# Performance work log

Hardware: AMD Instinct MI355X
Metric: run time of the kernel (lower is better)

The kernel has to match this reference:

```python
import jax, jax.numpy as jnp
import numpy as np


def setup_inputs() -> dict:
    key = jax.random.key(0)
    ks = jax.random.split(key, 9)
    B, S, D, E, I = 4, 2048, 1024, 8, 2048
    sd = 1.0 / np.sqrt(D)
    si = 1.0 / np.sqrt(I)
    return {
        "hidden_states": jax.random.normal(ks[0], (B, S, D), dtype=jnp.float32),
        "gate_w": jax.random.normal(ks[1], (D, E), dtype=jnp.float32) * sd,
        "expert_gate_w": jax.random.normal(ks[2], (E, D, I), dtype=jnp.float32) * sd,
        "expert_up_w": jax.random.normal(ks[3], (E, D, I), dtype=jnp.float32) * sd,
        "expert_down_w": jax.random.normal(ks[4], (E, I, D), dtype=jnp.float32) * si,
        "shared_gate_proj_w": jax.random.normal(ks[5], (D, I), dtype=jnp.float32) * sd,
        "shared_up_w": jax.random.normal(ks[6], (D, I), dtype=jnp.float32) * sd,
        "shared_down_w": jax.random.normal(ks[7], (I, D), dtype=jnp.float32) * si,
        "shared_expert_gate_w": jax.random.normal(ks[8], (D, 1), dtype=jnp.float32) * sd,
        "top_k": 2,
    }


def reference(hidden_states, gate_w, expert_gate_w, expert_up_w, expert_down_w,
              shared_gate_proj_w, shared_up_w, shared_down_w, shared_expert_gate_w,
              top_k):
    B, S, D = hidden_states.shape
    E = gate_w.shape[1]
    x = hidden_states.reshape(-1, D)            # [T, D]
    T = x.shape[0]

    # Router: softmax in fp32, top-k, dense per-token per-expert combine weights.
    gate_vals = x @ gate_w                      # [T, E]
    probs = jax.nn.softmax(gate_vals.astype(jnp.float32), axis=-1)
    top_w, top_i = jax.lax.top_k(probs, top_k)  # [T, K]
    dense_w = jnp.zeros((T, E), dtype=jnp.float32)
    dense_w = dense_w.at[jnp.arange(T)[:, None], top_i].set(top_w)
    dense_w = dense_w.astype(x.dtype)           # zero for unselected experts

    # All experts as batched SwiGLU GEMMs (tokens with zero weight contribute 0).
    g = jnp.einsum('td,edi->eti', x, expert_gate_w)
    u = jnp.einsum('td,edi->eti', x, expert_up_w)
    y = jnp.einsum('eti,eid->etd', jax.nn.silu(g) * u, expert_down_w)  # [E, T, D]
    moe_out = jnp.einsum('etd,te->td', y, dense_w)                      # [T, D]

    # Shared expert with sigmoid gate.
    shared = (jax.nn.silu(x @ shared_gate_proj_w) * (x @ shared_up_w)) @ shared_down_w
    shared = jax.nn.sigmoid(x @ shared_expert_gate_w) * shared

    final = (moe_out + shared).reshape(B, S, D)
    return final, gate_vals
```

## Files before the change

kernel.cpp:

```cpp
#include <hip/hip_runtime.h>

typedef __bf16 bf16x8 __attribute__((ext_vector_type(8)));
typedef float f32x4 __attribute__((ext_vector_type(4)));
typedef float f4 __attribute__((ext_vector_type(4)));
typedef unsigned short us8 __attribute__((ext_vector_type(8)));

#define T_TOK 8192
#define DDIM 1024
#define NEXP 8
#define IDIM 2048
#define NCH 1024
#define RROWS 17408
#define ROWS_TOT (T_TOK + RROWS)

__device__ __forceinline__ unsigned short f2bf(float f) {
    unsigned u = __float_as_uint(f);
    u += 0x7fffu + ((u >> 16) & 1u);
    return (unsigned short)(u >> 16);
}

__global__ __launch_bounds__(256) void router_kernel(
    const float* __restrict__ x, const float* __restrict__ gate_w,
    const float* __restrict__ sgw, float* __restrict__ gate_out,
    float* __restrict__ wdense, float* __restrict__ sgout)
{
    __shared__ float lgw[DDIM * NEXP];
    __shared__ float lsg[DDIM];
    int tid = threadIdx.x;
    for (int i = tid; i < (DDIM * NEXP) / 4; i += 256)
        ((f4*)lgw)[i] = ((const f4*)gate_w)[i];
    for (int i = tid; i < DDIM / 4; i += 256)
        ((f4*)lsg)[i] = ((const f4*)sgw)[i];
    __syncthreads();

    int wid = tid >> 6, l = tid & 63;
    int t = blockIdx.x * 4 + wid;

    float acc[NEXP];
#pragma unroll
    for (int e = 0; e < NEXP; e++) acc[e] = 0.f;
    float accs = 0.f;
    const float* xr = x + (size_t)t * DDIM;
#pragma unroll
    for (int j = 0; j < 4; j++) {
        int d0 = j * 256 + l * 4;
        f4 xv = *(const f4*)(xr + d0);
#pragma unroll
        for (int c = 0; c < 4; c++) {
            float xd = xv[c];
            int d = d0 + c;
#pragma unroll
            for (int e = 0; e < NEXP; e++) acc[e] += xd * lgw[d * NEXP + e];
            accs += xd * lsg[d];
        }
    }
#pragma unroll
    for (int off = 32; off > 0; off >>= 1) {
#pragma unroll
        for (int e = 0; e < NEXP; e++) acc[e] += __shfl_xor(acc[e], off);
        accs += __shfl_xor(accs, off);
    }
    if (l == 0) {
        float m = acc[0];
        for (int e = 1; e < NEXP; e++) m = fmaxf(m, acc[e]);
        float p[NEXP], s = 0.f;
        for (int e = 0; e < NEXP; e++) { p[e] = __expf(acc[e] - m); s += p[e]; }
        float inv = 1.f / s;
        int i1 = 0; float b1 = p[0];
        for (int e = 1; e < NEXP; e++) if (p[e] > b1) { b1 = p[e]; i1 = e; }
        int i2 = -1; float b2 = -1.f;
        for (int e = 0; e < NEXP; e++) if (e != i1 && p[e] > b2) { b2 = p[e]; i2 = e; }
        for (int e = 0; e < NEXP; e++) {
            gate_out[(size_t)t * NEXP + e] = acc[e];
            float w = (e == i1) ? b1 * inv : (e == i2) ? b2 * inv : 0.f;
            wdense[(size_t)t * NEXP + e] = w;
        }
        sgout[t] = 1.f / (1.f + __expf(-accs));
    }
}

__global__ __launch_bounds__(256) void bucket_kernel(
    const float* __restrict__ wdense, int* __restrict__ list,
    float* __restrict__ wl, int* __restrict__ cnt,
    int* __restrict__ te, int* __restrict__ tp)
{
    int e = blockIdx.x;
    int tid = threadIdx.x, wid = tid >> 6, l = tid & 63;
    __shared__ int wsum[4];
    int base = 0;
    int* le = list + (size_t)e * T_TOK;
    float* we = wl + (size_t)e * T_TOK;
    for (int t0 = 0; t0 < T_TOK; t0 += 256) {
        int tok = t0 + tid;
        float w = wdense[(size_t)tok * NEXP + e];
        bool f = w > 0.f;
        unsigned long long m = __ballot(f);
        int lp = __popcll(m & ((1ull << l) - 1ull));
        if (l == 0) wsum[wid] = __popcll(m);
        __syncthreads();
        int woff = 0;
#pragma unroll
        for (int i = 0; i < 4; i++) if (i < wid) woff += wsum[i];
        int btot = wsum[0] + wsum[1] + wsum[2] + wsum[3];
        if (f) {
            int pos = base + woff + lp;
            le[pos] = tok; we[pos] = w;
            int slot = 0;
            for (int e2 = 0; e2 < e; e2++)
                slot += (wdense[(size_t)tok * NEXP + e2] > 0.f) ? 1 : 0;
            te[tok * 2 + slot] = e;
            tp[tok * 2 + slot] = pos;
        }
        base += btot;
        __syncthreads();
    }
    if (tid == 0) cnt[e] = base;
    int align = (base + 127) & ~127;
    for (int i = base + tid; i < align; i += 256) { le[i] = 0; we[i] = 0.f; }
}

__global__ void scan_kernel(const int* __restrict__ cnt, int* __restrict__ offs)
{
    if (threadIdx.x == 0) {
        int o = 0;
        for (int e = 0; e < NEXP; e++) { offs[e] = o; o += (cnt[e] + 127) & ~127; }
    }
}

__global__ __launch_bounds__(256) void cvt_kernel(
    const float* __restrict__ in, unsigned short* __restrict__ out, int n8)
{
    int i = blockIdx.x * 256 + threadIdx.x;
    if (i >= n8) return;
    const f4* p = (const f4*)in + (size_t)i * 2;
    f4 a = p[0], b = p[1];
    us8 o;
#pragma unroll
    for (int k = 0; k < 4; k++) { o[k] = f2bf(a[k]); o[4 + k] = f2bf(b[k]); }
    *((us8*)out + i) = o;
}

__global__ __launch_bounds__(256) void wcvt_gu_kernel(
    const float* __restrict__ egw, const float* __restrict__ euw,
    const float* __restrict__ sgp, const float* __restrict__ sup,
    unsigned short* __restrict__ pool, int c0)
{
    int j = blockIdx.y;
    int e = j >> 1, s = j & 1;
    const float* src = (e < 8) ? ((s ? euw : egw) + (size_t)e * DDIM * IDIM)
                               : (s ? sup : sgp);
    unsigned short* dst = pool + (size_t)j * NCH * DDIM;
    int tpc = NCH / 64;
    int tci = blockIdx.x % tpc, tri = blockIdx.x / tpc;
    int r0 = tri * 64;
    int cl0 = tci * 64;
    int cg0 = c0 + cl0;

    __shared__ unsigned short lds[64][72];
    int t = threadIdx.x;
    int tr = t >> 4, tcc = (t & 15) * 4;
#pragma unroll
    for (int jj = 0; jj < 4; jj++) {
        int r = tr + jj * 16;
        f4 v = *(const f4*)(src + (size_t)(r0 + r) * IDIM + cg0 + tcc);
#pragma unroll
        for (int k = 0; k < 4; k++) lds[r][tcc + k] = f2bf(v[k]);
    }
    __syncthreads();
    int orow = t >> 2, ss = t & 3;
    us8 v0, v1;
#pragma unroll
    for (int i = 0; i < 8; i++) {
        v0[i] = lds[ss * 16 + i][orow];
        v1[i] = lds[ss * 16 + 8 + i][orow];
    }
    unsigned short* op = dst + (size_t)(cl0 + orow) * DDIM + r0 + ss * 16;
    *(us8*)op = v0; *(us8*)(op + 8) = v1;
}

__global__ __launch_bounds__(256) void wcvt_d_kernel(
    const float* __restrict__ edw, const float* __restrict__ sdw,
    unsigned short* __restrict__ pool)
{
    int j = blockIdx.y;
    const float* src = (j < 8) ? edw + (size_t)j * IDIM * DDIM : sdw;
    unsigned short* dst = pool + (size_t)j * DDIM * IDIM;
    int tpc = DDIM / 64;
    int tci = blockIdx.x % tpc, tri = blockIdx.x / tpc;
    int rg0 = tri * 64;
    int cg0 = tci * 64;

    __shared__ unsigned short lds[64][72];
    int t = threadIdx.x;
    int tr = t >> 4, tcc = (t & 15) * 4;
#pragma unroll
    for (int jj = 0; jj < 4; jj++) {
        int r = tr + jj * 16;
        f4 v = *(const f4*)(src + (size_t)(rg0 + r) * DDIM + cg0 + tcc);
#pragma unroll
        for (int k = 0; k < 4; k++) lds[r][tcc + k] = f2bf(v[k]);
    }
    __syncthreads();
    int orow = t >> 2, ss = t & 3;
    us8 v0, v1;
#pragma unroll
    for (int i = 0; i < 8; i++) {
        v0[i] = lds[ss * 16 + i][orow];
        v1[i] = lds[ss * 16 + 8 + i][orow];
    }
    unsigned short* op = dst + (size_t)(cg0 + orow) * IDIM + rg0 + ss * 16;
    *(us8*)op = v0; *(us8*)(op + 8) = v1;
}

__device__ __forceinline__ void stage_tile(
    const unsigned short* __restrict__ g, int row0, int ldk, int k0,
    unsigned short* lds, int wid, int lane)
{
#pragma unroll
    for (int j = 0; j < 2; j++) {
        int c = wid + j * 4;
        int seg = c * 64 + lane;
        int row = seg >> 2, ks = seg & 3;
        const unsigned short* gp = g + (size_t)(row0 + row) * ldk + k0 + ks * 8;
        __builtin_amdgcn_global_load_lds(
            (const __attribute__((address_space(1))) void*)gp,
            (__attribute__((address_space(3))) void*)(lds + c * 512),
            16, 0, 0);
    }
}

__global__ __launch_bounds__(256, 2) void gemm_gateup(
    const unsigned short* __restrict__ A, const unsigned short* __restrict__ pool,
    unsigned short* __restrict__ H, const int* __restrict__ listb,
    const int* __restrict__ cnt, const int* __restrict__ offs, int c0)
{
    int z = blockIdx.z;
    const unsigned short *Bg, *Bu; const int* lst; int count, rowb;
    if (z == 0) {
        Bg = pool + (size_t)16 * NCH * DDIM; Bu = pool + (size_t)17 * NCH * DDIM;
        lst = nullptr; count = T_TOK; rowb = 0;
    } else {
        int e = z - 1;
        Bg = pool + (size_t)(e * 2) * NCH * DDIM; Bu = pool + (size_t)(e * 2 + 1) * NCH * DDIM;
        lst = listb + (size_t)e * T_TOK; count = cnt[e]; rowb = T_TOK + offs[e];
    }
    int flat = blockIdx.y * 8 + blockIdx.x;
    int nt = flat & 7, mt = flat >> 3;
    int m0 = mt * 128, n0 = nt * 128;
    if (m0 >= count) return;
    const int K = DDIM;

    __shared__ unsigned short As[128 * 32], Bgs[128 * 32], Bus[128 * 32];
    int tid = threadIdx.x, wid = tid >> 6, l = tid & 63;
    int wm = wid >> 1, wn = wid & 1;
    int lr = l & 15, kg = l >> 4;

    int seg0 = wid * 64 + l, seg1 = (wid + 4) * 64 + l;
    int ra0 = seg0 >> 2, ka0 = seg0 & 3;
    int ra1 = seg1 >> 2, ka1 = seg1 & 3;
    int ga0 = lst ? lst[m0 + ra0] : (m0 + ra0);
    int ga1 = lst ? lst[m0 + ra1] : (m0 + ra1);
    const unsigned short* pa0 = A + (size_t)ga0 * K + ka0 * 8;
    const unsigned short* pa1 = A + (size_t)ga1 * K + ka1 * 8;

    f32x4 zero = {0.f, 0.f, 0.f, 0.f};
    f32x4 accg[4][4], accu[4][4];
#pragma unroll
    for (int m = 0; m < 4; m++)
#pragma unroll
        for (int n = 0; n < 4; n++) { accg[m][n] = zero; accu[m][n] = zero; }

    for (int k0 = 0; k0 < K; k0 += 32) {
        __builtin_amdgcn_global_load_lds(
            (const __attribute__((address_space(1))) void*)(pa0 + k0),
            (__attribute__((address_space(3))) void*)(As + wid * 512), 16, 0, 0);
        __builtin_amdgcn_global_load_lds(
            (const __attribute__((address_space(1))) void*)(pa1 + k0),
            (__attribute__((address_space(3))) void*)(As + (wid + 4) * 512), 16, 0, 0);
        stage_tile(Bg, n0, K, k0, Bgs, wid, l);
        stage_tile(Bu, n0, K, k0, Bus, wid, l);
        __syncthreads();
        bf16x8 a[4], bg[4], bu[4];
#pragma unroll
        for (int m = 0; m < 4; m++)
            a[m] = *(const bf16x8*)(As + ((wm * 64 + m * 16 + lr) * 32 + kg * 8));
#pragma unroll
        for (int n = 0; n < 4; n++) {
            bg[n] = *(const bf16x8*)(Bgs + ((wn * 64 + n * 16 + lr) * 32 + kg * 8));
            bu[n] = *(const bf16x8*)(Bus + ((wn * 64 + n * 16 + lr) * 32 + kg * 8));
        }
#pragma unroll
        for (int m = 0; m < 4; m++)
#pragma unroll
            for (int n = 0; n < 4; n++) {
                accg[m][n] = __builtin_amdgcn_mfma_f32_16x16x32_bf16(a[m], bg[n], accg[m][n], 0, 0, 0);
                accu[m][n] = __builtin_amdgcn_mfma_f32_16x16x32_bf16(a[m], bu[n], accu[m][n], 0, 0, 0);
            }
        __syncthreads();
    }

#pragma unroll
    for (int m = 0; m < 4; m++) {
        int row = rowb + m0 + wm * 64 + m * 16 + kg * 4;
#pragma unroll
        for (int n = 0; n < 4; n++) {
            int col = c0 + n0 + wn * 64 + n * 16 + lr;
#pragma unroll
            for (int r = 0; r < 4; r++) {
                float g = accg[m][n][r], u = accu[m][n][r];
                float hv = g * (1.f / (1.f + __expf(-g))) * u;
                H[(size_t)(row + r) * IDIM + col] = f2bf(hv);
            }
        }
    }
}

__global__ __launch_bounds__(256, 2) void gemm_down(
    const unsigned short* __restrict__ H, const unsigned short* __restrict__ pool,
    unsigned short* __restrict__ Y,
    const float* __restrict__ wlb, const float* __restrict__ sgo,
    const int* __restrict__ cnt, const int* __restrict__ offs)
{
    int z = blockIdx.z;
    const unsigned short* B; const float* coef; int count, rowb;
    if (z == 0) {
        B = pool + (size_t)8 * DDIM * IDIM;
        coef = sgo; count = T_TOK; rowb = 0;
    } else {
        int e = z - 1;
        B = pool + (size_t)e * DDIM * IDIM;
        coef = wlb + (size_t)e * T_TOK;
        count = cnt[e]; rowb = T_TOK + offs[e];
    }
    int flat = blockIdx.y * 8 + blockIdx.x;
    int nt = flat & 7, mt = flat >> 3;
    int m0 = mt * 128, n0 = nt * 128;
    if (m0 >= count) return;
    const unsigned short* Arows = H + (size_t)rowb * IDIM;

    __shared__ unsigned short As[128 * 32], Bs[128 * 32];
    int tid = threadIdx.x, wid = tid >> 6, l = tid & 63;
    int wm = wid >> 1, wn = wid & 1;
    int lr = l & 15, kg = l >> 4;

    f32x4 zero = {0.f, 0.f, 0.f, 0.f};
    f32x4 acc[4][4];
#pragma unroll
    for (int m = 0; m < 4; m++)
#pragma unroll
        for (int n = 0; n < 4; n++) acc[m][n] = zero;

    for (int k0 = 0; k0 < IDIM; k0 += 32) {
        stage_tile(Arows, m0, IDIM, k0, As, wid, l);
        stage_tile(B, n0, IDIM, k0, Bs, wid, l);
        __syncthreads();
        bf16x8 a[4], b[4];
#pragma unroll
        for (int m = 0; m < 4; m++)
            a[m] = *(const bf16x8*)(As + ((wm * 64 + m * 16 + lr) * 32 + kg * 8));
#pragma unroll
        for (int n = 0; n < 4; n++)
            b[n] = *(const bf16x8*)(Bs + ((wn * 64 + n * 16 + lr) * 32 + kg * 8));
#pragma unroll
        for (int m = 0; m < 4; m++)
#pragma unroll
            for (int n = 0; n < 4; n++)
                acc[m][n] = __builtin_amdgcn_mfma_f32_16x16x32_bf16(a[m], b[n], acc[m][n], 0, 0, 0);
        __syncthreads();
    }

#pragma unroll
    for (int m = 0; m < 4; m++) {
        int rloc = m0 + wm * 64 + m * 16 + kg * 4;
        float cf[4];
#pragma unroll
        for (int r = 0; r < 4; r++) cf[r] = coef[rloc + r];
#pragma unroll
        for (int n = 0; n < 4; n++) {
            int col = n0 + wn * 64 + n * 16 + lr;
#pragma unroll
            for (int r = 0; r < 4; r++)
                Y[(size_t)(rowb + rloc + r) * DDIM + col] = f2bf(cf[r] * acc[m][n][r]);
        }
    }
}

__global__ __launch_bounds__(256) void combine_kernel(
    const unsigned short* __restrict__ Y, const int* __restrict__ te,
    const int* __restrict__ tp, const int* __restrict__ offs,
    float* __restrict__ out)
{
    int t = blockIdx.x * 2 + (threadIdx.x >> 7);
    int c = (threadIdx.x & 127) * 8;
    int e0 = te[2 * t], e1 = te[2 * t + 1];
    size_t r0 = (size_t)T_TOK + offs[e0] + tp[2 * t];
    size_t r1 = (size_t)T_TOK + offs[e1] + tp[2 * t + 1];

    us8 vs = *(const us8*)(Y + (size_t)t * DDIM + c);
    us8 v0 = *(const us8*)(Y + r0 * DDIM + c);
    us8 v1 = *(const us8*)(Y + r1 * DDIM + c);
    f4 o0, o1;
#pragma unroll
    for (int k = 0; k < 4; k++) {
        o0[k] = __uint_as_float((unsigned)vs[k] << 16)
              + __uint_as_float((unsigned)v0[k] << 16)
              + __uint_as_float((unsigned)v1[k] << 16);
        o1[k] = __uint_as_float((unsigned)vs[4 + k] << 16)
              + __uint_as_float((unsigned)v0[4 + k] << 16)
              + __uint_as_float((unsigned)v1[4 + k] << 16);
    }
    float* op = out + (size_t)t * DDIM + c;
    *(f4*)op = o0;
    *(f4*)(op + 4) = o1;
}

extern "C" void kernel_launch(void* const* d_in, const int* in_sizes, int n_in,
                              void* d_out, int out_size, void* d_ws, size_t ws_size,
                              hipStream_t stream)
{
    const float* x   = (const float*)d_in[0];
    const float* gw  = (const float*)d_in[1];
    const float* egw = (const float*)d_in[2];
    const float* euw = (const float*)d_in[3];
    const float* edw = (const float*)d_in[4];
    const float* sgp = (const float*)d_in[5];
    const float* sup = (const float*)d_in[6];
    const float* sdw = (const float*)d_in[7];
    const float* seg = (const float*)d_in[8];

    float* out0 = (float*)d_out;
    float* gate_out = out0 + (size_t)T_TOK * DDIM;

    char* ws = (char*)d_ws;
    auto take = [&](size_t bytes) { char* p = ws; ws += (bytes + 255) & ~(size_t)255; return p; };
    unsigned short* xb   = (unsigned short*)take((size_t)T_TOK * DDIM * 2);
    float* wdense = (float*)take((size_t)T_TOK * NEXP * 4);
    float* sgo    = (float*)take((size_t)T_TOK * 4);
    int*   list   = (int*)take((size_t)NEXP * T_TOK * 4);
    float* wl     = (float*)take((size_t)NEXP * T_TOK * 4);
    int*   cnt    = (int*)take(256);
    int*   offs   = (int*)take(256);
    int*   te     = (int*)take((size_t)T_TOK * 2 * 4);
    int*   tp     = (int*)take((size_t)T_TOK * 2 * 4);
    unsigned short* pool = (unsigned short*)take((size_t)18 * NCH * DDIM * 2);
    unsigned short* H    = (unsigned short*)take((size_t)ROWS_TOT * IDIM * 2);
    unsigned short* Y    = (unsigned short*)take((size_t)ROWS_TOT * DDIM * 2);

    router_kernel<<<T_TOK / 4, 256, 0, stream>>>(x, gw, seg, gate_out, wdense, sgo);
    bucket_kernel<<<NEXP, 256, 0, stream>>>(wdense, list, wl, cnt, te, tp);
    scan_kernel<<<1, 64, 0, stream>>>(cnt, offs);
    cvt_kernel<<<(T_TOK * DDIM / 8) / 256, 256, 0, stream>>>(x, xb, T_TOK * DDIM / 8);

    for (int c = 0; c < 2; c++) {
        int c0 = c * NCH;
        wcvt_gu_kernel<<<dim3((NCH / 64) * 16, 18), 256, 0, stream>>>(
            egw, euw, sgp, sup, pool, c0);
        gemm_gateup<<<dim3(8, 64, 9), 256, 0, stream>>>(
            xb, pool, H, list, cnt, offs, c0);
    }

    wcvt_d_kernel<<<dim3((IDIM / 64) * 16, 9), 256, 0, stream>>>(edw, sdw, pool);
    gemm_down<<<dim3(8, 64, 9), 256, 0, stream>>>(H, pool, Y, wl, sgo, cnt, offs);

    combine_kernel<<<T_TOK / 2, 256, 0, stream>>>(Y, te, tp, offs, out0);
}
```

Baseline: 590.8 us.

## Fuse x bf16 conversion into router, drop scan kernel, unchunk gate/up weights

Writes the bf16 copy of x inside the router kernel, so the separate cvt pass and its extra read of x go away. The scan kernel is removed and each GEMM and the combine kernel recompute expert offsets from counts themselves. Gate/up weights are converted once at full IDIM width, and the gate-up GEMM runs as two launches (shared, then routed) instead of two chunked passes. The Y buffer now aliases the gate/up weight pool, and row guards are added on the stores. This cuts launch count and redundant memory traffic, at the cost of a larger weight workspace and a serialization between the shared and routed launches.

New measurement: 573.1 us. 3.0% less time.

```diff
diff --git a/kernel.cpp b/kernel.cpp
--- a/kernel.cpp
+++ b/kernel.cpp
@@ -4,12 +4,12 @@
 typedef float f32x4 __attribute__((ext_vector_type(4)));
 typedef float f4 __attribute__((ext_vector_type(4)));
 typedef unsigned short us8 __attribute__((ext_vector_type(8)));
+typedef unsigned short us4 __attribute__((ext_vector_type(4)));
 
 #define T_TOK 8192
 #define DDIM 1024
 #define NEXP 8
 #define IDIM 2048
-#define NCH 1024
 #define RROWS 17408
 #define ROWS_TOT (T_TOK + RROWS)
 
@@ -19,10 +19,21 @@
     return (unsigned short)(u >> 16);
 }
 
+#define GLDS(src, dst) __builtin_amdgcn_global_load_lds( \
+    (const __attribute__((address_space(1))) void*)(src), \
+    (__attribute__((address_space(3))) void*)(dst), 16, 0, 0)
+
+__device__ __forceinline__ int offs_of(const int* __restrict__ cnt, int e) {
+    int o = 0;
+    for (int i = 0; i < e; i++) o += (cnt[i] + 127) & ~127;
+    return o;
+}
+
 __global__ __launch_bounds__(256) void router_kernel(
     const float* __restrict__ x, const float* __restrict__ gate_w,
     const float* __restrict__ sgw, float* __restrict__ gate_out,
-    float* __restrict__ wdense, float* __restrict__ sgout)
+    float* __restrict__ wdense, float* __restrict__ sgout,
+    unsigned short* __restrict__ xb)
 {
     __shared__ float lgw[DDIM * NEXP];
     __shared__ float lsg[DDIM];
@@ -41,18 +52,22 @@
     for (int e = 0; e < NEXP; e++) acc[e] = 0.f;
     float accs = 0.f;
     const float* xr = x + (size_t)t * DDIM;
+    unsigned short* xbr = xb + (size_t)t * DDIM;
 #pragma unroll
     for (int j = 0; j < 4; j++) {
         int d0 = j * 256 + l * 4;
         f4 xv = *(const f4*)(xr + d0);
+        us4 xo;
 #pragma unroll
         for (int c = 0; c < 4; c++) {
             float xd = xv[c];
+            xo[c] = f2bf(xd);
             int d = d0 + c;
 #pragma unroll
             for (int e = 0; e < NEXP; e++) acc[e] += xd * lgw[d * NEXP + e];
             accs += xd * lsg[d];
         }
+        *(us4*)(xbr + d0) = xo;
     }
 #pragma unroll
     for (int off = 32; off > 0; off >>= 1) {
@@ -115,46 +130,24 @@
         __syncthreads();
     }
     if (tid == 0) cnt[e] = base;
-    int align = (base + 127) & ~127;
+    int align = (base + 255) & ~255;
     for (int i = base + tid; i < align; i += 256) { le[i] = 0; we[i] = 0.f; }
-}
-
-__global__ void scan_kernel(const int* __restrict__ cnt, int* __restrict__ offs)
-{
-    if (threadIdx.x == 0) {
-        int o = 0;
-        for (int e = 0; e < NEXP; e++) { offs[e] = o; o += (cnt[e] + 127) & ~127; }
-    }
-}
-
-__global__ __launch_bounds__(256) void cvt_kernel(
-    const float* __restrict__ in, unsigned short* __restrict__ out, int n8)
-{
-    int i = blockIdx.x * 256 + threadIdx.x;
-    if (i >= n8) return;
-    const f4* p = (const f4*)in + (size_t)i * 2;
-    f4 a = p[0], b = p[1];
-    us8 o;
-#pragma unroll
-    for (int k = 0; k < 4; k++) { o[k] = f2bf(a[k]); o[4 + k] = f2bf(b[k]); }
-    *((us8*)out + i) = o;
 }
 
 __global__ __launch_bounds__(256) void wcvt_gu_kernel(
     const float* __restrict__ egw, const float* __restrict__ euw,
     const float* __restrict__ sgp, const float* __restrict__ sup,
-    unsigned short* __restrict__ pool, int c0)
+    unsigned short* __restrict__ pool)
 {
     int j = blockIdx.y;
     int e = j >> 1, s = j & 1;
     const float* src = (e < 8) ? ((s ? euw : egw) + (size_t)e * DDIM * IDIM)
                                : (s ? sup : sgp);
-    unsigned short* dst = pool + (size_t)j * NCH * DDIM;
-    int tpc = NCH / 64;
+    unsigned short* dst = pool + (size_t)j * IDIM * DDIM;
+    int tpc = IDIM / 64;
     int tci = blockIdx.x % tpc, tri = blockIdx.x / tpc;
     int r0 = tri * 64;
-    int cl0 = tci * 64;
-    int cg0 = c0 + cl0;
+    int cg0 = tci * 64;
 
     __shared__ unsigned short lds[64][72];
     int t = threadIdx.x;
@@ -174,7 +167,7 @@
         v0[i] = lds[ss * 16 + i][orow];
         v1[i] = lds[ss * 16 + 8 + i][orow];
     }
-    unsigned short* op = dst + (size_t)(cl0 + orow) * DDIM + r0 + ss * 16;
+    unsigned short* op = dst + (size_t)(cg0 + orow) * DDIM + r0 + ss * 16;
     *(us8*)op = v0; *(us8*)(op + 8) = v1;
 }
 
@@ -222,32 +215,27 @@
         int seg = c * 64 + lane;
         int row = seg >> 2, ks = seg & 3;
         const unsigned short* gp = g + (size_t)(row0 + row) * ldk + k0 + ks * 8;
-        __builtin_amdgcn_global_load_lds(
-            (const __attribute__((address_space(1))) void*)gp,
-            (__attribute__((address_space(3))) void*)(lds + c * 512),
-            16, 0, 0);
-    }
-}
-
-__global__ __launch_bounds__(256, 2) void gemm_gateup(
+        GLDS(gp, lds + c * 512);
+    }
+}
+
+__global__ __launch_bounds__(256, 2) void gemm_gu128(
     const unsigned short* __restrict__ A, const unsigned short* __restrict__ pool,
     unsigned short* __restrict__ H, const int* __restrict__ listb,
-    const int* __restrict__ cnt, const int* __restrict__ offs, int c0)
-{
-    int z = blockIdx.z;
+    const int* __restrict__ cnt, int routed)
+{
     const unsigned short *Bg, *Bu; const int* lst; int count, rowb;
-    if (z == 0) {
-        Bg = pool + (size_t)16 * NCH * DDIM; Bu = pool + (size_t)17 * NCH * DDIM;
+    if (!routed) {
+        Bg = pool + (size_t)16 * IDIM * DDIM; Bu = pool + (size_t)17 * IDIM * DDIM;
         lst = nullptr; count = T_TOK; rowb = 0;
     } else {
-        int e = z - 1;
-        Bg = pool + (size_t)(e * 2) * NCH * DDIM; Bu = pool + (size_t)(e * 2 + 1) * NCH * DDIM;
-        lst = listb + (size_t)e * T_TOK; count = cnt[e]; rowb = T_TOK + offs[e];
-    }
-    int flat = blockIdx.y * 8 + blockIdx.x;
-    int nt = flat & 7, mt = flat >> 3;
-    int m0 = mt * 128, n0 = nt * 128;
+        int e = blockIdx.z;
+        Bg = pool + (size_t)(e * 2) * IDIM * DDIM; Bu = pool + (size_t)(e * 2 + 1) * IDIM * DDIM;
+        lst = listb + (size_t)e * T_TOK; count = cnt[e]; rowb = T_TOK + offs_of(cnt, e);
+    }
+    int m0 = blockIdx.y * 128, n0 = blockIdx.x * 128;
     if (m0 >= count) return;
+    int climit = (count + 127) & ~127;
     const int K = DDIM;
 
     __shared__ unsigned short As[128 * 32], Bgs[128 * 32], Bus[128 * 32];
@@ -271,12 +259,8 @@
         for (int n = 0; n < 4; n++) { accg[m][n] = zero; accu[m][n] = zero; }
 
     for (int k0 = 0; k0 < K; k0 += 32) {
-        __builtin_amdgcn_global_load_lds(
-            (const __attribute__((address_space(1))) void*)(pa0 + k0),
-            (__attribute__((address_space(3))) void*)(As + wid * 512), 16, 0, 0);
-        __builtin_amdgcn_global_load_lds(
-            (const __attribute__((address_space(1))) void*)(pa1 + k0),
-            (__attribute__((address_space(3))) void*)(As + (wid + 4) * 512), 16, 0, 0);
+        GLDS(pa0 + k0, As + wid * 512);
+        GLDS(pa1 + k0, As + (wid + 4) * 512);
         stage_tile(Bg, n0, K, k0, Bgs, wid, l);
         stage_tile(Bu, n0, K, k0, Bus, wid, l);
         __syncthreads();
@@ -301,41 +285,43 @@
 
 #pragma unroll
     for (int m = 0; m < 4; m++) {
-        int row = rowb + m0 + wm * 64 + m * 16 + kg * 4;
+        int rbase = m0 + wm * 64 + m * 16 + kg * 4;
 #pragma unroll
         for (int n = 0; n < 4; n++) {
-            int col = c0 + n0 + wn * 64 + n * 16 + lr;
+            int col = n0 + wn * 64 + n * 16 + lr;
 #pragma unroll
             for (int r = 0; r < 4; r++) {
-                float g = accg[m][n][r], u = accu[m][n][r];
-                float hv = g * (1.f / (1.f + __expf(-g))) * u;
-                H[(size_t)(row + r) * IDIM + col] = f2bf(hv);
+                int rloc = rbase + r;
+                if (rloc < climit) {
+                    float g = accg[m][n][r], u = accu[m][n][r];
+                    float hv = g * (1.f / (1.f + __expf(-g))) * u;
+                    H[(size_t)(rowb + rloc) * IDIM + col] = f2bf(hv);
+                }
             }
         }
     }
 }
 
-__global__ __launch_bounds__(256, 2) void gemm_down(
-    const unsigned short* __restrict__ H, const unsigned short* __restrict__ pool,
+__global__ __launch_bounds__(256, 2) void gemm_dn128(
+    const unsigned short* __restrict__ H, const unsigned short* __restrict__ wd,
     unsigned short* __restrict__ Y,
     const float* __restrict__ wlb, const float* __restrict__ sgo,
-    const int* __restrict__ cnt, const int* __restrict__ offs)
+    const int* __restrict__ cnt)
 {
     int z = blockIdx.z;
     const unsigned short* B; const float* coef; int count, rowb;
     if (z == 0) {
-        B = pool + (size_t)8 * DDIM * IDIM;
+        B = wd + (size_t)8 * DDIM * IDIM;
         coef = sgo; count = T_TOK; rowb = 0;
     } else {
         int e = z - 1;
-        B = pool + (size_t)e * DDIM * IDIM;
+        B = wd + (size_t)e * DDIM * IDIM;
         coef = wlb + (size_t)e * T_TOK;
-        count = cnt[e]; rowb = T_TOK + offs[e];
-    }
-    int flat = blockIdx.y * 8 + blockIdx.x;
-    int nt = flat & 7, mt = flat >> 3;
-    int m0 = mt * 128, n0 = nt * 128;
+        count = cnt[e]; rowb = T_TOK + offs_of(cnt, e);
+    }
+    int m0 = blockIdx.y * 128, n0 = blockIdx.x * 128;
     if (m0 >= count) return;
+    int climit = (count + 127) & ~127;
     const unsigned short* Arows = H + (size_t)rowb * IDIM;
 
     __shared__ unsigned short As[128 * 32], Bs[128 * 32];
@@ -371,30 +357,42 @@
 
 #pragma unroll
     for (int m = 0; m < 4; m++) {
-        int rloc = m0 + wm * 64 + m * 16 + kg * 4;
+        int rbase = m0 + wm * 64 + m * 16 + kg * 4;
         float cf[4];
 #pragma unroll
-        for (int r = 0; r < 4; r++) cf[r] = coef[rloc + r];
+        for (int r = 0; r < 4; r++) {
+            int rloc = rbase + r;
+            cf[r] = (rloc < climit) ? coef[rloc] : 0.f;
+        }
 #pragma unroll
         for (int n = 0; n < 4; n++) {
             int col = n0 + wn * 64 + n * 16 + lr;
 #pragma unroll
-            for (int r = 0; r < 4; r++)
-                Y[(size_t)(rowb + rloc + r) * DDIM + col] = f2bf(cf[r] * acc[m][n][r]);
+            for (int r = 0; r < 4; r++) {
+                int rloc = rbase + r;
+                if (rloc < climit)
+                    Y[(size_t)(rowb + rloc) * DDIM + col] = f2bf(cf[r] * acc[m][n][r]);
+            }
         }
     }
 }
 
 __global__ __launch_bounds__(256) void combine_kernel(
     const unsigned short* __restrict__ Y, const int* __restrict__ te,
-    const int* __restrict__ tp, const int* __restrict__ offs,
+    const int* __restrict__ tp, const int* __restrict__ cnt,
     float* __restrict__ out)
 {
+    int off[NEXP];
+    {
+        int o = 0;
+#pragma unroll
+        for (int i = 0; i < NEXP; i++) { off[i] = o; o += (cnt[i] + 127) & ~127; }
+    }
     int t = blockIdx.x * 2 + (threadIdx.x >> 7);
     int c = (threadIdx.x & 127) * 8;
     int e0 = te[2 * t], e1 = te[2 * t + 1];
-    size_t r0 = (size_t)T_TOK + offs[e0] + tp[2 * t];
-    size_t r1 = (size_t)T_TOK + offs[e1] + tp[2 * t + 1];
+    size_t r0 = (size_t)T_TOK + off[e0] + tp[2 * t];
+    size_t r1 = (size_t)T_TOK + off[e1] + tp[2 * t + 1];
 
     us8 vs = *(const us8*)(Y + (size_t)t * DDIM + c);
     us8 v0 = *(const us8*)(Y + r0 * DDIM + c);
@@ -439,28 +437,28 @@
     int*   list   = (int*)take((size_t)NEXP * T_TOK * 4);
     float* wl     = (float*)take((size_t)NEXP * T_TOK * 4);
     int*   cnt    = (int*)take(256);
-    int*   offs   = (int*)take(256);
     int*   te     = (int*)take((size_t)T_TOK * 2 * 4);
     int*   tp     = (int*)take((size_t)T_TOK * 2 * 4);
-    unsigned short* pool = (unsigned short*)take((size_t)18 * NCH * DDIM * 2);
-    unsigned short* H    = (unsigned short*)take((size_t)ROWS_TOT * IDIM * 2);
-    unsigned short* Y    = (unsigned short*)take((size_t)ROWS_TOT * DDIM * 2);
-
-    router_kernel<<<T_TOK / 4, 256, 0, stream>>>(x, gw, seg, gate_out, wdense, sgo);
+    unsigned short* guPool = (unsigned short*)take((size_t)18 * IDIM * DDIM * 2);
+    unsigned short* wdPool = (unsigned short*)take((size_t)9 * DDIM * IDIM * 2);
+    unsigned short* H      = (unsigned short*)take((size_t)ROWS_TOT * IDIM * 2);
+    unsigned short* Y      = guPool;
+
+    router_kernel<<<T_TOK / 4, 256, 0, stream>>>(x, gw, seg, gate_out, wdense, sgo, xb);
     bucket_kernel<<<NEXP, 256, 0, stream>>>(wdense, list, wl, cnt, te, tp);
-    scan_kernel<<<1, 64, 0, stream>>>(cnt, offs);
-    cvt_kernel<<<(T_TOK * DDIM / 8) / 256, 256, 0, stream>>>(x, xb, T_TOK * DDIM / 8);
-
-    for (int c = 0; c < 2; c++) {
-        int c0 = c * NCH;
-        wcvt_gu_kernel<<<dim3((NCH / 64) * 16, 18), 256, 0, stream>>>(
-            egw, euw, sgp, sup, pool, c0);
-        gemm_gateup<<<dim3(8, 64, 9), 256, 0, stream>>>(
-            xb, pool, H, list, cnt, offs, c0);
-    }
-
-    wcvt_d_kernel<<<dim3((IDIM / 64) * 16, 9), 256, 0, stream>>>(edw, sdw, pool);
-    gemm_down<<<dim3(8, 64, 9), 256, 0, stream>>>(H, pool, Y, wl, sgo, cnt, offs);
-
-    combine_kernel<<<T_TOK / 2, 256, 0, stream>>>(Y, te, tp, offs, out0);
-}
+
+    wcvt_gu_kernel<<<dim3((IDIM / 64) * (DDIM / 64), 18), 256, 0, stream>>>(
+        egw, euw, sgp, sup, guPool);
+
+    gemm_gu128<<<dim3(IDIM / 128, T_TOK / 128), 256, 0, stream>>>(
+        xb, guPool, H, list, cnt, 0);
+    gemm_gu128<<<dim3(IDIM / 128, T_TOK / 128, NEXP), 256, 0, stream>>>(
+        xb, guPool, H, list, cnt, 1);
+
+    wcvt_d_kernel<<<dim3((DDIM / 64) * (IDIM / 64), 9), 256, 0, stream>>>(
+        edw, sdw, wdPool);
+    gemm_dn128<<<dim3(DDIM / 128, T_TOK / 128, 9), 256, 0, stream>>>(
+        H, wdPool, Y, wl, sgo, cnt);
+
+    combine_kernel<<<T_TOK / 2, 256, 0, stream>>>(Y, te, tp, cnt, out0);
+}
```
